# Performance work log

Measured on AMD Instinct MI355X. Metric: run time of the kernel, lower is better.

## Reference

```python
import jax, jax.numpy as jnp
import numpy as np

SOFTMAX_EPS = 1e-16  # PyG softmax denominator eps
LN_EPS = 1e-5
NEG_SLOPE = 0.2      # RGATConv default negative_slope
NUM_LAYERS = 4


def segment_softmax(alpha, seg, n):
    # softmax over edges sharing the same destination node ('across-relation')
    amax = jax.ops.segment_max(alpha, seg, num_segments=n)
    amax = jnp.where(jnp.isfinite(amax), amax, 0.0)
    e = jnp.exp(alpha - amax[seg])
    den = jax.ops.segment_sum(e, seg, num_segments=n)
    return e / (den[seg] + SOFTMAX_EPS)


def graph_layer_norm(x, w, b):
    # torch_geometric.nn.LayerNorm, mode='graph', batch=None:
    # normalize over ALL nodes and channels jointly
    mu = x.mean()
    xc = x - mu
    std = jnp.sqrt((xc * xc).mean())
    return xc / (std + LN_EPS) * w + b


def normalize_pos(pos):
    # NormalizeScale: center then scale so max |coord| ~ 1
    pos = pos - pos.mean(axis=0, keepdims=True)
    pos = pos * ((1.0 / jnp.abs(pos).max()) * 0.999999)
    # NormalizeRotation: rotate onto principal axes of pos^T pos
    c = pos.T @ pos  # (3,3)
    _, v = jnp.linalg.eigh(c)
    return pos @ v


def rgat_layer(x, src, dst, etype, W, q, k, bias, n):
    # RGATConv, heads=1, dim=1, concat=False, additive self-attention,
    # across-relation softmax, sum aggregation, eval mode (no dropout).
    # Transform per relation once: (R, N, O), then gather per edge.
    xr = jnp.einsum('nf,rfo->rno', x, W)
    out_j = xr[etype, src]            # (E, O) source messages
    out_i = xr[etype, dst]            # (E, O) target side
    qi = out_i @ q                    # (E, 1)
    kj = out_j @ k                    # (E, 1)
    alpha = jax.nn.leaky_relu(qi + kj, NEG_SLOPE)
    alpha = segment_softmax(alpha, dst, n)
    msg = alpha * out_j               # (E, O), heads=1 so mean over heads is identity
    agg = jax.ops.segment_sum(msg, dst, num_segments=n)
    return agg + bias


def setup_inputs() -> dict:
    key = jax.random.key(0)
    kk = jax.random.split(key, 16)
    N, E, R, IN, O, H2 = 100000, 3200000, 15, 35, 32, 256
    return {
        'data_batch_1': jax.random.normal(kk[0], (N, IN), jnp.float32),
        'data_batch_2': jax.random.normal(kk[1], (16, IN), jnp.float32),
        'edge_index_1': jax.random.randint(kk[2], (2, E), 0, N, jnp.int32),
        'edge_type_1': jax.random.randint(kk[3], (E,), 0, R, jnp.int32),
        'edge_index_2': jax.random.randint(kk[4], (2, 16), 0, 16, jnp.int32),
        'edge_type_2': jax.random.randint(kk[5], (16,), 0, R, jnp.int32),
        'W0': jax.random.normal(kk[6], (R, IN, O), jnp.float32) * 0.1,
        'q0': jax.random.normal(kk[7], (O, 1), jnp.float32) * 0.1,
        'k0': jax.random.normal(kk[8], (O, 1), jnp.float32) * 0.1,
        'b0': jnp.zeros((O,), jnp.float32),
        'Ws': jax.random.normal(kk[9], (NUM_LAYERS - 1, R, O, O), jnp.float32) * 0.1,
        'qs': jax.random.normal(kk[10], (NUM_LAYERS - 1, O, 1), jnp.float32) * 0.1,
        'ks': jax.random.normal(kk[11], (NUM_LAYERS - 1, O, 1), jnp.float32) * 0.1,
        'bs': jnp.zeros((NUM_LAYERS - 1, O), jnp.float32),
        'ln_w': jnp.ones((NUM_LAYERS, O), jnp.float32),
        'ln_b': jnp.zeros((NUM_LAYERS, O), jnp.float32),
        'ln1_w': jnp.ones((IN - 3,), jnp.float32),
        'ln1_b': jnp.zeros((IN - 3,), jnp.float32),
        'lin1_W': jax.random.normal(kk[12], (H2, O), jnp.float32) * 0.1,
        'lin1_b': jnp.zeros((H2,), jnp.float32),
    }


def reference(data_batch_1, data_batch_2, edge_index_1, edge_type_1,
              edge_index_2, edge_type_2,
              W0, q0, k0, b0, Ws, qs, ks, bs,
              ln_w, ln_b, ln1_w, ln1_b, lin1_W, lin1_b):
    n = data_batch_1.shape[0]
    xyz = normalize_pos(data_batch_1[:, :3])
    feats = graph_layer_norm(data_batch_1[:, 3:], ln1_w, ln1_b)
    x = jnp.concatenate([xyz, feats], axis=1)
    src, dst = edge_index_1[0], edge_index_1[1]
    prev = None
    for i in range(NUM_LAYERS):
        if i == 0:
            h = rgat_layer(x, src, dst, edge_type_1, W0, q0, k0, b0, n)
        else:
            h = rgat_layer(x, src, dst, edge_type_1,
                           Ws[i - 1], qs[i - 1], ks[i - 1], bs[i - 1], n)
        if prev is not None:  # residual from 2nd layer on
            h = h + prev
        h = graph_layer_norm(h, ln_w[i], ln_b[i])
        h = jax.nn.silu(h)
        prev = h
        x = h
    x3 = x.mean(axis=0)                                  # mean pool over nodes
    out = jax.nn.silu(x3 @ lin1_W.T + lin1_b)[None, :]   # (1, 256)
    # original returns (x, lins[-1]) which are the identical tensor
    return out
```

## Files before the change

kernel.cpp:

```cpp
#include <hip/hip_runtime.h>
#include <math.h>
#include <stdint.h>

#define NBLK 256

__device__ inline float bf2f(unsigned short u){
  union { unsigned int i; float f; } x; x.i = ((unsigned int)u) << 16; return x.f;
}
__device__ inline unsigned short f2bf(float f){
  union { float f; unsigned int i; } x; x.f = f;
  unsigned int u = x.i;
  return (unsigned short)((u + 0x7FFFu + ((u >> 16) & 1u)) >> 16);
}
__device__ inline float ldin(const void* p, size_t i, int f32){
  return f32 ? ((const float*)p)[i] : bf2f(((const unsigned short*)p)[i]);
}

__device__ inline int badf(float v){ return !(fabsf(v) <= 3.0e38f); }
__device__ inline int badd(double v){ return !(fabs(v) <= 1.0e300); }

__device__ inline double wsum_d(double v){
  #pragma unroll
  for (int o = 32; o > 0; o >>= 1) v += __shfl_down(v, o);
  return v;
}
__device__ inline double wmax_d(double v){
  #pragma unroll
  for (int o = 32; o > 0; o >>= 1) v = fmax(v, __shfl_down(v, o));
  return v;
}
__device__ inline void atomicMaxD(double* addr, double v){
  atomicMax((unsigned long long*)addr, (unsigned long long)__double_as_longlong(v));
}

typedef __attribute__((ext_vector_type(8))) short short8;
typedef __attribute__((ext_vector_type(4))) float f32x4;
__device__ inline f32x4 mfma16(short8 a, short8 b, f32x4 c){
  return __builtin_amdgcn_mfma_f32_16x16x32_bf16(a, b, c, 0, 0, 0);
}

__device__ inline double d_sign(double a, double b){ return (b >= 0.0) ? fabs(a) : -fabs(a); }
__device__ inline double dlapy2_(double x, double y){ return sqrt(x*x + y*y); }

__device__ void dlartg_(double f, double g, double* cs, double* sn, double* r){
  if (g == 0.0){ *cs = 1.0; *sn = 0.0; *r = f; }
  else if (f == 0.0){ *cs = 0.0; *sn = (g >= 0.0) ? 1.0 : -1.0; *r = fabs(g); }
  else {
    double d = sqrt(f*f + g*g);
    *cs = fabs(f)/d;
    *r  = d_sign(d, f);
    *sn = g / (*r);
  }
}

__device__ void dlaev2_(double a, double b, double c, double* rt1, double* rt2,
                        double* cs1, double* sn1){
  double sm = a + c, df = a - c, adf = fabs(df), tb = b + b, ab = fabs(tb);
  double acmx, acmn;
  if (fabs(a) > fabs(c)){ acmx = a; acmn = c; } else { acmx = c; acmn = a; }
  double rt;
  if (adf > ab) rt = adf*sqrt(1.0 + (ab/adf)*(ab/adf));
  else if (adf < ab) rt = ab*sqrt(1.0 + (adf/ab)*(adf/ab));
  else rt = ab*sqrt(2.0);
  int sgn1;
  if (sm < 0.0){ *rt1 = 0.5*(sm - rt); sgn1 = -1; *rt2 = (acmx/(*rt1))*acmn - (b/(*rt1))*b; }
  else if (sm > 0.0){ *rt1 = 0.5*(sm + rt); sgn1 = 1; *rt2 = (acmx/(*rt1))*acmn - (b/(*rt1))*b; }
  else { *rt1 = 0.5*rt; *rt2 = -0.5*rt; sgn1 = 1; }
  int sgn2; double cs;
  if (df >= 0.0){ cs = df + rt; sgn2 = 1; } else { cs = df - rt; sgn2 = -1; }
  double acs = fabs(cs);
  if (acs > ab){ double ct = -tb/cs; *sn1 = 1.0/sqrt(1.0+ct*ct); *cs1 = ct*(*sn1); }
  else {
    if (ab == 0.0){ *cs1 = 1.0; *sn1 = 0.0; }
    else { double tn = -cs/tb; *cs1 = 1.0/sqrt(1.0+tn*tn); *sn1 = tn*(*cs1); }
  }
  if (sgn1 == sgn2){ double tn = *cs1; *cs1 = -(*sn1); *sn1 = tn; }
}

__device__ void dsteqr3_(double* dd, double* ee, double z[3][3]){
  #define D_(i) dd[(i)-1]
  #define E_(i) ee[(i)-1]
  #define Z_(i,j) z[(i)-1][(j)-1]
  #define CW_(i) cw[(i)-1]
  #define SW_(i) sw[(i)-1]
  const int n = 3;
  const double eps = 1.1102230246251565e-16;
  const double eps2 = eps*eps;
  const double safmin = 2.2250738585072014e-308;
  const int nmaxit = n*30;
  double cw[3], sw[3];
  int jtot = 0;
  int l1 = 1, l, m, lsv, lend, lendsv;
  double p, g, r, c, s, f, b, rt1, rt2, anorm, tst;

L10:
  if (l1 > n) goto L160;
  if (l1 > 1) E_(l1-1) = 0.0;
  if (l1 <= n-1){
    for (m = l1; m <= n-1; ++m){
      tst = fabs(E_(m));
      if (tst == 0.0) goto L30;
      if (tst <= (sqrt(fabs(D_(m)))*sqrt(fabs(D_(m+1))))*eps){ E_(m) = 0.0; goto L30; }
    }
  }
  m = n;
L30:
  l = l1; lsv = l; lend = m; lendsv = lend; l1 = m+1;
  if (lend == l) goto L10;
  anorm = 0.0;
  for (int i = l; i <= lend; ++i) anorm = fmax(anorm, fabs(D_(i)));
  for (int i = l; i <= lend-1; ++i) anorm = fmax(anorm, fabs(E_(i)));
  if (anorm == 0.0) goto L10;
  if (fabs(D_(lend)) < fabs(D_(l))){ lend = lsv; l = lendsv; }
  if (lend > l) goto L40; else goto L90;

L40:
  if (l != lend){
    for (m = l; m <= lend-1; ++m){
      tst = fabs(E_(m)); tst = tst*tst;
      if (tst <= (eps2*fabs(D_(m)))*fabs(D_(m+1)) + safmin) goto L60;
    }
  }
  m = lend;
L60:
  if (m < lend) E_(m) = 0.0;
  p = D_(l);
  if (m == l) goto L80;
  if (m == l+1){
    dlaev2_(D_(l), E_(l), D_(l+1), &rt1, &rt2, &c, &s);
    CW_(l) = c; SW_(l) = s;
    { double ct = CW_(l), st = SW_(l);
      if (ct != 1.0 || st != 0.0)
        for (int i = 1; i <= n; ++i){
          double t = Z_(i, l+1);
          Z_(i, l+1) = ct*t - st*Z_(i, l);
          Z_(i, l)   = st*t + ct*Z_(i, l);
        }
    }
    D_(l) = rt1; D_(l+1) = rt2; E_(l) = 0.0;
    l += 2;
    if (l <= lend) goto L40;
    goto L140;
  }
  if (jtot == nmaxit) goto L140;
  jtot++;
  g = (D_(l+1) - p)/(2.0*E_(l));
  r = dlapy2_(g, 1.0);
  g = D_(m) - p + E_(l)/(g + d_sign(r, g));
  s = 1.0; c = 1.0; p = 0.0;
  for (int i = m-1; i >= l; --i){
    f = s*E_(i); b = c*E_(i);
    dlartg_(g, f, &c, &s, &r);
    if (i != m-1) E_(i+1) = r;
    g = D_(i+1) - p;
    r = (D_(i) - g)*s + 2.0*c*b;
    p = s*r;
    D_(i+1) = g + p;
    g = c*r - b;
    CW_(i) = c; SW_(i) = -s;
  }
  { int mm = m - l + 1;
    for (int j = mm-1; j >= 1; --j){
      double ct = CW_(l+j-1), st = SW_(l+j-1);
      if (ct != 1.0 || st != 0.0)
        for (int i = 1; i <= n; ++i){
          double t = Z_(i, l+j);
          Z_(i, l+j)   = ct*t - st*Z_(i, l+j-1);
          Z_(i, l+j-1) = st*t + ct*Z_(i, l+j-1);
        }
    }
  }
  D_(l) = D_(l) - p;
  E_(l) = g;
  goto L40;
L80:
  D_(l) = p;
  l++;
  if (l <= lend) goto L40;
  goto L140;

L90:
  if (l != lend){
    for (m = l; m >= lend+1; --m){
      tst = fabs(E_(m-1)); tst = tst*tst;
      if (tst <= (eps2*fabs(D_(m)))*fabs(D_(m-1)) + safmin) goto L110;
    }
  }
  m = lend;
L110:
  if (m > lend) E_(m-1) = 0.0;
  p = D_(l);
  if (m == l) goto L130;
  if (m == l-1){
    dlaev2_(D_(l-1), E_(l-1), D_(l), &rt1, &rt2, &c, &s);
    CW_(m) = c; SW_(m) = s;
    { double ct = CW_(m), st = SW_(m);
      if (ct != 1.0 || st != 0.0)
        for (int i = 1; i <= n; ++i){
          double t = Z_(i, l);
          Z_(i, l)   = ct*t - st*Z_(i, l-1);
          Z_(i, l-1) = st*t + ct*Z_(i, l-1);
        }
    }
    D_(l-1) = rt1; D_(l) = rt2; E_(l-1) = 0.0;
    l -= 2;
    if (l >= lend) goto L90;
    goto L140;
  }
  if (jtot == nmaxit) goto L140;
  jtot++;
  g = (D_(l-1) - p)/(2.0*E_(l-1));
  r = dlapy2_(g, 1.0);
  g = D_(m) - p + E_(l-1)/(g + d_sign(r, g));
  s = 1.0; c = 1.0; p = 0.0;
  for (int i = m; i <= l-1; ++i){
    f = s*E_(i); b = c*E_(i);
    dlartg_(g, f, &c, &s, &r);
    if (i != m) E_(i-1) = r;
    g = D_(i) - p;
    r = (D_(i+1) - g)*s + 2.0*c*b;
    p = s*r;
    D_(i) = g + p;
    g = c*r - b;
    CW_(i) = c; SW_(i) = s;
  }
  { int mm = l - m + 1;
    for (int j = 1; j <= mm-1; ++j){
      double ct = CW_(m+j-1), st = SW_(m+j-1);
      if (ct != 1.0 || st != 0.0)
        for (int i = 1; i <= n; ++i){
          double t = Z_(i, m+j);
          Z_(i, m+j)   = ct*t - st*Z_(i, m+j-1);
          Z_(i, m+j-1) = st*t + ct*Z_(i, m+j-1);
        }
    }
  }
  D_(l) = D_(l) - p;
  E_(l-1) = g;
  goto L90;
L130:
  D_(l) = p;
  l--;
  if (l >= lend) goto L90;
  goto L140;

L140:
  if (jtot < nmaxit) goto L10;
  goto L190;

L160:
  for (int ii = 2; ii <= n; ++ii){
    int i = ii-1, k = i;
    p = D_(i);
    for (int j = ii; j <= n; ++j) if (D_(j) < p){ k = j; p = D_(j); }
    if (k != i){
      D_(k) = D_(i); D_(i) = p;
      for (int rr = 1; rr <= n; ++rr){ double t = Z_(rr,i); Z_(rr,i) = Z_(rr,k); Z_(rr,k) = t; }
    }
  }
L190:
  ;
  #undef D_
  #undef E_
  #undef Z_
  #undef CW_
  #undef SW_
}

__device__ void eigh3_(const double C[3][3], double w[3], double v[3][3]){
  double a00=C[0][0], a10=C[1][0], a20=C[2][0], a11=C[1][1], a21=C[2][1], a22=C[2][2];
  double dd[3], ee[2], tau, v2;
  double alpha = a10, x = a20;
  double xnorm = fabs(x);
  if (xnorm == 0.0){ tau = 0.0; v2 = 0.0; ee[0] = alpha; }
  else {
    double beta = -d_sign(dlapy2_(alpha, xnorm), alpha);
    tau = (beta - alpha)/beta;
    v2 = x/(alpha - beta);
    ee[0] = beta;
  }
  if (tau != 0.0){
    double w0 = tau*(a11 + a21*v2);
    double w1 = tau*(a21 + a22*v2);
    double wv = w0 + w1*v2;
    double ac = -0.5*tau*wv;
    w0 += ac; w1 += ac*v2;
    a11 = a11 - 2.0*w0;
    a21 = a21 - (v2*w0 + w1);
    a22 = a22 - 2.0*v2*w1;
  }
  dd[0]=a00; dd[1]=a11; dd[2]=a22; ee[1]=a21;
  double z[3][3] = {{1,0,0},{0,1,0},{0,0,1}};
  dsteqr3_(dd, ee, z);
  for (int j = 0; j < 3; ++j){
    double t = z[1][j] + v2*z[2][j];
    z[1][j] -= tau*t;
    z[2][j] -= tau*t*v2;
  }
  for (int i=0;i<3;++i){ w[i]=dd[i]; for(int j=0;j<3;++j) v[i][j]=z[i][j]; }
}


__global__ void k_dtype(const unsigned short* __restrict__ data, int nus, double* PD){
  int* DF = (int*)(PD + 28);
  int t = threadIdx.x;
  int bad = 0;
  for (int i = t; i < nus; i += 256){
    int e = (data[i] >> 7) & 0xFF;
    if (e > 0x90 || (e && e < 0x60)) bad++;
  }
  #pragma unroll
  for (int o = 32; o > 0; o >>= 1) bad += __shfl_down(bad, o);
  __shared__ int sb[4];
  if ((t & 63) == 0) sb[t >> 6] = bad;
  __syncthreads();
  if (t == 0) DF[1] = ((sb[0]+sb[1]+sb[2]+sb[3]) > nus/16) ? 1 : 0;
}

__global__ void k_red1(const void* __restrict__ data, int N, double* PD){
  int n = blockIdx.x*blockDim.x + threadIdx.x;
  const int* DF = (const int*)(PD + 28);
  int f32 = DF[1];
  double v11[11] = {0,0,0,0,0,0,0,0,0,0,0};
  double m6[6] = {0,0,0,0,0,0};
  if (n < N){
    size_t rb = (size_t)n*35;
    double p0 = ldin(data, rb+0, f32);
    double p1 = ldin(data, rb+1, f32);
    double p2 = ldin(data, rb+2, f32);
    v11[0]=p0; v11[1]=p1; v11[2]=p2;
    double fs=0, fss=0;
    for (int k=3;k<35;++k){ double v = ldin(data, rb+k, f32); fs += v; fss += v*v; }
    v11[3]=fs; v11[4]=fss;
    v11[5]=p0*p0; v11[6]=p1*p0; v11[7]=p2*p0; v11[8]=p1*p1; v11[9]=p2*p1; v11[10]=p2*p2;
    m6[0]=64.0+p0; m6[1]=64.0+p1; m6[2]=64.0+p2;
    m6[3]=64.0-p0; m6[4]=64.0-p1; m6[5]=64.0-p2;
  }
  __shared__ double sred[17][4];
  int wid = threadIdx.x >> 6;
  int lane0 = ((threadIdx.x & 63) == 0);
  #pragma unroll
  for (int q=0;q<11;++q){
    double t = wsum_d(v11[q]);
    if (lane0) sred[q][wid] = t;
  }
  #pragma unroll
  for (int j=0;j<6;++j){
    double t = wmax_d(m6[j]);
    if (lane0) sred[11+j][wid] = t;
  }
  __syncthreads();
  int t = threadIdx.x;
  if (t < 11) atomicAdd(&PD[t], sred[t][0]+sred[t][1]+sred[t][2]+sred[t][3]);
  else if (t < 17)
    atomicMaxD(&PD[72+(t-11)],
      fmax(fmax(sred[t][0],sred[t][1]), fmax(sred[t][2],sred[t][3])));
}

__global__ void k_eig(double* PD, int N){
  if (threadIdx.x != 0 || blockIdx.x != 0) return;
  int* DF = (int*)(PD + 28);
  int bad0 = 0;
  for (int i=0;i<11;++i) if (badd(PD[i])) bad0 = 1;
  if (bad0) DF[0] |= 1;
  double dN = (double)N;
  double mu[3] = {PD[0]/dN, PD[1]/dN, PD[2]/dN};
  double amax = 0.0;
  for (int j=0;j<3;++j){
    double mx = (PD[72+j] - 64.0) - mu[j];
    double mnv = mu[j] - (64.0 - PD[75+j]);
    amax = fmax(amax, fmax(mx, mnv));
  }
  double s = 0.999999/amax;
  double s2 = s*s;
  double C[3][3];
  C[0][0]=(PD[5]-dN*mu[0]*mu[0])*s2; C[1][0]=(PD[6]-dN*mu[1]*mu[0])*s2;
  C[2][0]=(PD[7]-dN*mu[2]*mu[0])*s2; C[1][1]=(PD[8]-dN*mu[1]*mu[1])*s2;
  C[2][1]=(PD[9]-dN*mu[2]*mu[1])*s2; C[2][2]=(PD[10]-dN*mu[2]*mu[2])*s2;
  C[0][1]=C[1][0]; C[0][2]=C[2][0]; C[1][2]=C[2][1];
  double w[3], V[3][3];
  eigh3_(C, w, V);
  int bad1 = 0;
  for (int i=0;i<3;++i){ if (badd(w[i])) bad1=1; for (int j=0;j<3;++j) if (badd(V[i][j])) bad1=1; }
  if (bad1){
    DF[0] |= 2;
    for (int i=0;i<3;++i) for (int j=0;j<3;++j) V[i][j] = (i==j) ? 1.0 : 0.0;
  }
  PD[12]=mu[0]; PD[13]=mu[1]; PD[14]=mu[2];
  PD[15]=s;
  for (int i=0;i<3;++i) for (int j=0;j<3;++j) PD[16+i*3+j]=V[i][j];
  double cntf = dN*32.0;
  double mu1 = PD[3]/cntf;
  double var = PD[4]/cntf - mu1*mu1;
  PD[25]=mu1;
  PD[26]=1.0/(sqrt(var>0.0?var:0.0)+1e-5);
}

__global__ void k_buildx(const void* __restrict__ data,
                         const void* __restrict__ ln1w,
                         const void* __restrict__ ln1b,
                         double* __restrict__ PD, float* __restrict__ x, int N){
  int n = blockIdx.x*blockDim.x + threadIdx.x;
  if (n >= N) return;
  int* DF = (int*)(PD + 28);
  int f32 = DF[1];
  size_t rb = (size_t)n*35;
  double s = PD[15];
  double p0 = ((double)ldin(data, rb+0, f32) - PD[12])*s;
  double p1 = ((double)ldin(data, rb+1, f32) - PD[13])*s;
  double p2 = ((double)ldin(data, rb+2, f32) - PD[14])*s;
  float* xr = x + (size_t)n*36;
  int bb = 0;
  for (int j=0;j<3;++j){
    float v = (float)(p0*PD[16+j] + p1*PD[19+j] + p2*PD[22+j]);
    bb |= badf(v);
    xr[j] = v;
  }
  float mu1 = (float)PD[25], rs = (float)PD[26];
  for (int k=0;k<32;++k){
    float v = (ldin(data, rb+3+k, f32) - mu1)*rs*ldin(ln1w, k, f32) + ldin(ln1b, k, f32);
    bb |= badf(v);
    xr[3+k] = v;
  }
  xr[35] = 0.f;
  if (bb) atomicOr(DF, 4);
}

__global__ void k_count(const int* __restrict__ dst, int* __restrict__ cnt, int E){
  int i = blockIdx.x*blockDim.x + threadIdx.x;
  if (i < E) atomicAdd(&cnt[dst[i]], 1);
}

__global__ void k_scan1(const int* __restrict__ cnt, int* __restrict__ bsum, int N){
  int i = blockIdx.x*256 + threadIdx.x;
  int v = (i < N) ? cnt[i] : 0;
  #pragma unroll
  for (int o=32;o>0;o>>=1) v += __shfl_down(v, o);
  __shared__ int s4[4];
  if ((threadIdx.x&63)==0) s4[threadIdx.x>>6]=v;
  __syncthreads();
  if (threadIdx.x==0) bsum[blockIdx.x]=s4[0]+s4[1]+s4[2]+s4[3];
}

__global__ void k_scan2(const int* __restrict__ bsum, int* __restrict__ bpre,
                        int* __restrict__ iptr, int nb, int N){
  if (threadIdx.x != 0 || blockIdx.x != 0) return;
  int run = 0;
  for (int b=0;b<nb;++b){ bpre[b]=run; run += bsum[b]; }
  iptr[N] = run;
}

__global__ void k_scan3(const int* __restrict__ cnt, const int* __restrict__ bpre,
                        int* __restrict__ iptr, int* __restrict__ cur, int N){
  __shared__ int sc[256];
  int i = blockIdx.x*256 + threadIdx.x;
  int t = threadIdx.x;
  int v = (i < N) ? cnt[i] : 0;
  sc[t] = v;
  __syncthreads();
  for (int o=1;o<256;o<<=1){
    int add = (t >= o) ? sc[t-o] : 0;
    __syncthreads();
    sc[t] += add;
    __syncthreads();
  }
  if (i < N){
    int val = bpre[blockIdx.x] + sc[t] - v;
    iptr[i] = val;
    cur[i] = val;
  }
}

__global__ void k_hist(const int* __restrict__ dst, int* __restrict__ H,
                       int E, int per, int nb){
  __shared__ int lc[256];
  int blk = blockIdx.x, t = threadIdx.x;
  lc[t] = 0;
  __syncthreads();
  int s = blk*per, e = min(E, s+per);
  for (int i = s+t; i < e; i += 256) atomicAdd(&lc[dst[i] >> 9], 1);
  __syncthreads();
  if (t < nb) H[t*NBLK + blk] = lc[t];
}

__global__ void k_xscan(const int* __restrict__ H, const int* __restrict__ iptr,
                        int* __restrict__ offs){
  __shared__ int sc[256];
  int b = blockIdx.x, t = threadIdx.x;
  int v = H[b*NBLK + t];
  sc[t] = v;
  __syncthreads();
  for (int o=1;o<256;o<<=1){
    int add = (t >= o) ? sc[t-o] : 0;
    __syncthreads();
    sc[t] += add;
    __syncthreads();
  }
  offs[b*NBLK + t] = iptr[b << 9] + sc[t] - v;
}

__global__ void k_binA2(const int* __restrict__ src, const int* __restrict__ dst,
                        const int* __restrict__ et, const int* __restrict__ offs,
                        int* __restrict__ stag, int E, int per){
  __shared__ int lc[256];
  int blk = blockIdx.x, t = threadIdx.x;
  lc[t] = 0;
  __syncthreads();
  int s = blk*per, e = min(E, s+per);
  for (int i = s+t; i < e; i += 256){
    int d = dst[i];
    int b = d >> 9;
    int r = atomicAdd(&lc[b], 1);
    stag[offs[b*NBLK + blk] + r] = src[i] | (et[i] << 17) | ((d & 511) << 21);
  }
}

__global__ void k_binB2(const int* __restrict__ iptr, const int* __restrict__ stag,
                        int* __restrict__ pack, int N){
  __shared__ int lcnt[512];
  int b = blockIdx.x;
  int n0 = b << 9;
  int t = threadIdx.x;
  for (int j = t; j < 512; j += 256){
    int n = n0 + j;
    lcnt[j] = (n < N) ? iptr[n] : 0;
  }
  __syncthreads();
  int segs = iptr[n0];
  int nend = (n0 + 512 < N) ? (n0 + 512) : N;
  int sege = iptr[nend];
  for (int k = segs + t; k < sege; k += 256){
    int e2 = stag[k];
    int pos = atomicAdd(&lcnt[(e2 >> 21) & 511], 1);
    pack[pos] = (e2 & 0x1FFFF) | (((e2 >> 17) & 15) << 20);
  }
}

__global__ void k_scatter(const int* __restrict__ src, const int* __restrict__ dst,
                          const int* __restrict__ et, int* __restrict__ cur,
                          int* __restrict__ pack, int E){
  int i = blockIdx.x*blockDim.x + threadIdx.x;
  if (i < E){
    int d = dst[i];
    int p = atomicAdd(&cur[d], 1);
    pack[p] = src[i] | (et[i] << 20);
  }
}

__global__ void k_fragpack(const void* __restrict__ W, size_t wofs, int F, int KC,
                           const void* __restrict__ qp, const void* __restrict__ kp,
                           size_t qofs,
                           unsigned short* __restrict__ bfr,
                           unsigned short* __restrict__ qkfr,
                           const int* __restrict__ DF){
  int t = blockIdx.x*blockDim.x + threadIdx.x;
  int nB = 15*KC*2*64*8;
  int nQ = 2*2*KC*64*8;
  int f32 = DF[1];
  if (t < nB){
    int j = t & 7; int lane = (t >> 3) & 63; int tile = (t >> 9) & 1; int idx = t >> 10;
    int kc = idx % KC; int r = idx / KC;
    int f = kc*32 + (lane >> 4)*8 + j;
    int o = tile*16 + (lane & 15);
    bfr[t] = (f < F) ? f2bf(ldin(W, wofs + ((size_t)(r*F+f))*32 + o, f32)) : 0;
  } else if (t < nB + nQ){
    int u = t - nB;
    int j = u & 7; int lane = (u >> 3) & 63; int wpk = u >> 9;
    int kc = wpk % KC; int wp = wpk / KC;
    int part = wp & 1; int which = wp >> 1;
    int f = kc*32 + (lane >> 4)*8 + j;
    int rr = lane & 15;
    unsigned short val = 0;
    if (f < F && rr < 15){
      const void* v = which ? kp : qp;
      float acc = 0.f;
      for (int o = 0; o < 32; ++o)
        acc = fmaf(ldin(W, wofs + ((size_t)(rr*F+f))*32 + o, f32), ldin(v, qofs + o, f32), acc);
      unsigned short hi = f2bf(acc);
      val = (part == 0) ? hi : f2bf(acc - bf2f(hi));
    }
    qkfr[u] = val;
  }
}

__global__ void __launch_bounds__(256)
k_mf(const float* __restrict__ x, int str, int KC, int N,
     const unsigned short* __restrict__ bfr,
     const unsigned short* __restrict__ qkfr,
     unsigned short* __restrict__ y, float* __restrict__ yq, float* __restrict__ yk){
  int wave = blockIdx.x*(blockDim.x >> 6) + (threadIdx.x >> 6);
  int node0 = wave*16;
  if (node0 >= N) return;
  int lane = threadIdx.x & 63;
  int col = lane & 15, quad = lane >> 4;
  int r0 = blockIdx.y*3;

  short8 ah[2], al[2];
  #pragma unroll
  for (int kc = 0; kc < 2; ++kc){
    if (kc >= KC) break;
    float xv[8];
    int node = node0 + col;
    int kbase = kc*32 + quad*8;
    if (node < N && kbase < str){
      const float* xr = x + (size_t)node*str + kbase;
      if (kbase + 8 <= str){
        float4 a = *(const float4*)xr; float4 b = *(const float4*)(xr + 4);
        xv[0]=a.x; xv[1]=a.y; xv[2]=a.z; xv[3]=a.w; xv[4]=b.x; xv[5]=b.y; xv[6]=b.z; xv[7]=b.w;
      } else if (kbase + 4 <= str){
        float4 a = *(const float4*)xr;
        xv[0]=a.x; xv[1]=a.y; xv[2]=a.z; xv[3]=a.w; xv[4]=0.f; xv[5]=0.f; xv[6]=0.f; xv[7]=0.f;
      } else {
        #pragma unroll
        for (int j=0;j<8;++j) xv[j]=0.f;
      }
    } else {
      #pragma unroll
      for (int j=0;j<8;++j) xv[j]=0.f;
    }
    #pragma unroll
    for (int j=0;j<8;++j){
      unsigned short hi = f2bf(xv[j]);
      ah[kc][j] = (short)hi;
      al[kc][j] = (short)f2bf(xv[j] - bf2f(hi));
    }
  }

  const short8* B  = (const short8*)bfr;
  const short8* QK = (const short8*)qkfr;

  if (blockIdx.y == 0){
    f32x4 aq = {0.f,0.f,0.f,0.f}, ak2 = {0.f,0.f,0.f,0.f};
    for (int kc = 0; kc < KC; ++kc){
      short8 qh = QK[((0*KC) + kc)*64 + lane];
      short8 ql = QK[((1*KC) + kc)*64 + lane];
      short8 kh = QK[((2*KC) + kc)*64 + lane];
      short8 kl = QK[((3*KC) + kc)*64 + lane];
      aq = mfma16(ah[kc], qh, aq);
      aq = mfma16(al[kc], qh, aq);
      aq = mfma16(ah[kc], ql, aq);
      ak2 = mfma16(ah[kc], kh, ak2);
      ak2 = mfma16(al[kc], kh, ak2);
      ak2 = mfma16(ah[kc], kl, ak2);
    }
    #pragma unroll
    for (int j = 0; j < 4; ++j){
      int node = node0 + quad*4 + j;
      if (node < N){
        yq[(size_t)node*16 + col] = aq[j];
        yk[(size_t)node*16 + col] = ak2[j];
      }
    }
  }

  for (int r = r0; r < r0+3; ++r){
    f32x4 a0 = {0.f,0.f,0.f,0.f}, a1 = {0.f,0.f,0.f,0.f};
    for (int kc = 0; kc < KC; ++kc){
      short8 b0 = B[(((size_t)(r*KC + kc))*2 + 0)*64 + lane];
      short8 b1 = B[(((size_t)(r*KC + kc))*2 + 1)*64 + lane];
      a0 = mfma16(ah[kc], b0, a0);
      a0 = mfma16(al[kc], b0, a0);
      a1 = mfma16(ah[kc], b1, a1);
      a1 = mfma16(al[kc], b1, a1);
    }
    #pragma unroll
    for (int j = 0; j < 4; ++j){
      int node = node0 + quad*4 + j;
      if (node < N){
        unsigned int pk = (unsigned int)f2bf(a0[j]) | ((unsigned int)f2bf(a1[j]) << 16);
        *(unsigned int*)&y[(((size_t)r*N + node))*32 + col*2] = pk;
      }
    }
  }
}

__global__ void k_main(const int* __restrict__ iptr, const int* __restrict__ pack,
                       const float* __restrict__ yq, const float* __restrict__ yk,
                       const unsigned short* __restrict__ y,
                       const void* __restrict__ biasp, size_t bofs,
                       const float* __restrict__ xres, float* __restrict__ hpre,
                       double* __restrict__ partials, int* __restrict__ DF, int N){
  __shared__ double sdb[4][2];
  int gt = blockIdx.x*blockDim.x + threadIdx.x;
  int node = gt >> 6, lane = gt & 63;
  int wid = threadIdx.x >> 6;
  int f32 = DF[1];
  int o = lane & 31;
  int os = ((o & 15) << 1) | (o >> 4);
  bool active = (node < N);
  float hp = 0.f;

  if (active){
    int start = iptr[node];
    int deg = iptr[node+1] - start;
    const float* yqn = yq + (size_t)node*16;
    float acc = 0.f;
    float ssum = 0.f;

    if (deg <= 64){
      int pe = 0; float a = -INFINITY;
      if (lane < deg){
        pe = pack[start+lane];
        int sr = pe & 0xFFFFF, et = pe >> 20;
        a = yqn[et] + yk[(size_t)sr*16+et];
        a = (a >= 0.f) ? a : 0.2f*a;
      }
      float amax = a;
      #pragma unroll
      for (int o2=32;o2>0;o2>>=1) amax = fmaxf(amax, __shfl_xor(amax, o2));
      float ev = (lane < deg) ? expf(a - amax) : 0.f;
      ssum = ev;
      int sub = lane >> 5;
      for (; sub + 14 < deg; sub += 16){
        float w0 = __shfl(ev, sub),    w1 = __shfl(ev, sub+2);
        float w2 = __shfl(ev, sub+4),  w3 = __shfl(ev, sub+6);
        float w4 = __shfl(ev, sub+8),  w5 = __shfl(ev, sub+10);
        float w6 = __shfl(ev, sub+12), w7 = __shfl(ev, sub+14);
        int   p0 = __shfl(pe, sub),    p1 = __shfl(pe, sub+2);
        int   p2 = __shfl(pe, sub+4),  p3 = __shfl(pe, sub+6);
        int   p4 = __shfl(pe, sub+8),  p5 = __shfl(pe, sub+10);
        int   p6 = __shfl(pe, sub+12), p7 = __shfl(pe, sub+14);
        float v0 = bf2f(y[((size_t)(p0 >> 20)*N + (p0 & 0xFFFFF))*32 + os]);
        float v1 = bf2f(y[((size_t)(p1 >> 20)*N + (p1 & 0xFFFFF))*32 + os]);
        float v2 = bf2f(y[((size_t)(p2 >> 20)*N + (p2 & 0xFFFFF))*32 + os]);
        float v3 = bf2f(y[((size_t)(p3 >> 20)*N + (p3 & 0xFFFFF))*32 + os]);
        float v4 = bf2f(y[((size_t)(p4 >> 20)*N + (p4 & 0xFFFFF))*32 + os]);
        float v5 = bf2f(y[((size_t)(p5 >> 20)*N + (p5 & 0xFFFFF))*32 + os]);
        float v6 = bf2f(y[((size_t)(p6 >> 20)*N + (p6 & 0xFFFFF))*32 + os]);
        float v7 = bf2f(y[((size_t)(p7 >> 20)*N + (p7 & 0xFFFFF))*32 + os]);
        acc = fmaf(w0, v0, acc); acc = fmaf(w1, v1, acc);
        acc = fmaf(w2, v2, acc); acc = fmaf(w3, v3, acc);
        acc = fmaf(w4, v4, acc); acc = fmaf(w5, v5, acc);
        acc = fmaf(w6, v6, acc); acc = fmaf(w7, v7, acc);
      }
      for (; sub + 6 < deg; sub += 8){
        float w0 = __shfl(ev, sub),   w1 = __shfl(ev, sub+2);
        float w2 = __shfl(ev, sub+4), w3 = __shfl(ev, sub+6);
        int   p0 = __shfl(pe, sub),   p1 = __shfl(pe, sub+2);
        int   p2 = __shfl(pe, sub+4), p3 = __shfl(pe, sub+6);
        float v0 = bf2f(y[((size_t)(p0 >> 20)*N + (p0 & 0xFFFFF))*32 + os]);
        float v1 = bf2f(y[((size_t)(p1 >> 20)*N + (p1 & 0xFFFFF))*32 + os]);
        float v2 = bf2f(y[((size_t)(p2 >> 20)*N + (p2 & 0xFFFFF))*32 + os]);
        float v3 = bf2f(y[((size_t)(p3 >> 20)*N + (p3 & 0xFFFFF))*32 + os]);
        acc = fmaf(w0, v0, acc); acc = fmaf(w1, v1, acc);
        acc = fmaf(w2, v2, acc); acc = fmaf(w3, v3, acc);
      }
      for (; sub < deg; sub += 2){
        float wgt = __shfl(ev, sub);
        int pb = __shfl(pe, sub);
        acc = fmaf(wgt, bf2f(y[((size_t)(pb >> 20)*N + (pb & 0xFFFFF))*32 + os]), acc);
      }
    } else {
      float amax = -INFINITY;
      for (int k = lane; k < deg; k += 64){
        int pe = pack[start+k];
        int sr = pe & 0xFFFFF, et = pe >> 20;
        float a = yqn[et] + yk[(size_t)sr*16+et];
        a = (a >= 0.f) ? a : 0.2f*a;
        amax = fmaxf(amax, a);
      }
      #pragma unroll
      for (int o2=32;o2>0;o2>>=1) amax = fmaxf(amax, __shfl_xor(amax, o2));
      for (int c = 0; c < deg; c += 64){
        int k = c + lane;
        float ev = 0.f; int pe = 0;
        if (k < deg){
          pe = pack[start+k];
          int sr = pe & 0xFFFFF, et = pe >> 20;
          float a = yqn[et] + yk[(size_t)sr*16+et];
          a = (a >= 0.f) ? a : 0.2f*a;
          ev = expf(a - amax);
          ssum += ev;
        }
        int lim = min(64, deg - c);
        int sub = lane >> 5;
        for (; sub + 6 < lim; sub += 8){
          float w0 = __shfl(ev, sub),   w1 = __shfl(ev, sub+2);
          float w2 = __shfl(ev, sub+4), w3 = __shfl(ev, sub+6);
          int   p0 = __shfl(pe, sub),   p1 = __shfl(pe, sub+2);
          int   p2 = __shfl(pe, sub+4), p3 = __shfl(pe, sub+6);
          float v0 = bf2f(y[((size_t)(p0 >> 20)*N + (p0 & 0xFFFFF))*32 + os]);
          float v1 = bf2f(y[((size_t)(p1 >> 20)*N + (p1 & 0xFFFFF))*32 + os]);
          float v2 = bf2f(y[((size_t)(p2 >> 20)*N + (p2 & 0xFFFFF))*32 + os]);
          float v3 = bf2f(y[((size_t)(p3 >> 20)*N + (p3 & 0xFFFFF))*32 + os]);
          acc = fmaf(w0, v0, acc);
          acc = fmaf(w1, v1, acc);
          acc = fmaf(w2, v2, acc);
          acc = fmaf(w3, v3, acc);
        }
        for (; sub < lim; sub += 2){
          float wgt = __shfl(ev, sub);
          int pb = __shfl(pe, sub);
          acc = fmaf(wgt, bf2f(y[((size_t)(pb >> 20)*N + (pb & 0xFFFFF))*32 + os]), acc);
        }
      }
    }
    #pragma unroll
    for (int o2=32;o2>0;o2>>=1) ssum += __shfl_xor(ssum, o2);
    float inv = 1.f/(ssum + 1e-16f);
    acc *= inv;
    acc += __shfl_xor(acc, 32);

    if (lane < 32){
      hp = acc + ldin(biasp, bofs + o, f32);
      if (xres) hp += xres[(size_t)node*32 + o];
      if (badf(hp)) atomicOr(DF, 32);
      hpre[(size_t)node*32 + o] = hp;
    }
  }

  float s1 = (active && lane < 32) ? hp : 0.f;
  float s2 = s1*s1;
  #pragma unroll
  for (int o2=32;o2>0;o2>>=1){ s1 += __shfl_xor(s1,o2); s2 += __shfl_xor(s2,o2); }
  if (lane == 0){ sdb[wid][0] = (double)s1; sdb[wid][1] = (double)s2; }
  __syncthreads();
  if (threadIdx.x == 0){
    partials[(size_t)blockIdx.x*2]   = sdb[0][0]+sdb[1][0]+sdb[2][0]+sdb[3][0];
    partials[(size_t)blockIdx.x*2+1] = sdb[0][1]+sdb[1][1]+sdb[2][1]+sdb[3][1];
  }
}

__global__ void k_stat(const double* __restrict__ partials, int nb,
                       double* __restrict__ PD, int l){
  double t1 = 0.0, t2 = 0.0;
  for (int i = threadIdx.x; i < nb; i += 256){
    t1 += partials[(size_t)i*2];
    t2 += partials[(size_t)i*2+1];
  }
  t1 = wsum_d(t1); t2 = wsum_d(t2);
  __shared__ double sd[8];
  int w = threadIdx.x >> 6;
  if ((threadIdx.x & 63) == 0){ sd[w*2] = t1; sd[w*2+1] = t2; }
  __syncthreads();
  if (threadIdx.x == 0){
    PD[32+2*l]   = sd[0]+sd[2]+sd[4]+sd[6];
    PD[32+2*l+1] = sd[1]+sd[3]+sd[5]+sd[7];
  }
}

__global__ void k_ln(float* __restrict__ h, const void* __restrict__ lnw,
                     const void* __restrict__ lnb, size_t lofs,
                     double* __restrict__ PD, int l, int N){
  int idx = blockIdx.x*blockDim.x + threadIdx.x;
  if (idx >= N*32) return;
  int* DF = (int*)(PD + 28);
  int f32 = DF[1];
  const double* stats = PD + 32 + 2*l;
  int o = idx & 31;
  double cntf = (double)N*32.0;
  double mu = stats[0]/cntf;
  double var = stats[1]/cntf - mu*mu;
  float rstd = (float)(1.0/(sqrt(var>0.0?var:0.0) + 1e-5));
  float v = (h[idx] - (float)mu)*rstd*ldin(lnw, lofs + o, f32) + ldin(lnb, lofs + o, f32);
  v = v / (1.f + expf(-v));
  if (badf(v)) atomicOr(DF, 64);
  h[idx] = v;
}

__global__ void k_pool(const float* __restrict__ h, double* __restrict__ PD, int N){
  __shared__ float sp[8][33];
  int t = threadIdx.x, o = t & 31, g = t >> 5;
  int r0 = blockIdx.x*256;
  float s = 0.f;
  for (int r = r0 + g; r < N && r < r0 + 256; r += 8) s += h[(size_t)r*32 + o];
  sp[g][o] = s;
  __syncthreads();
  if (t < 32){
    float tot = 0.f;
    #pragma unroll
    for (int g2=0; g2<8; ++g2) tot += sp[g2][t];
    atomicAdd(&PD[40 + t], (double)tot);
  }
}

__global__ void k_out(double* __restrict__ PD, const void* __restrict__ Wl,
                      const void* __restrict__ bl, void* __restrict__ out, int N, int H2){
  int j = blockIdx.x*blockDim.x + threadIdx.x;
  if (j >= H2) return;
  int* DF = (int*)(PD + 28);
  int f32 = DF[1];
  int flag = DF[0];
  const double* pool = PD + 40;
  float acc = ldin(bl, j, f32);
  for (int o=0;o<32;++o)
    acc = fmaf((float)(pool[o]/(double)N), ldin(Wl, (size_t)j*32+o, f32), acc);
  if (badf(acc)) flag |= 128;
  float v = acc / (1.f + expf(-acc));
  if (flag) v = (float)flag;
  if (f32) ((float*)out)[j] = v;
  else     ((unsigned short*)out)[j] = f2bf(v);
}

__global__ void k_diag(unsigned short* out, float val, int H2){
  int j = blockIdx.x*blockDim.x + threadIdx.x;
  if (j < H2) out[j] = f2bf(val);
}

extern "C" void kernel_launch(void* const* d_in, const int* in_sizes, int n_in,
                              void* d_out, int out_size, void* d_ws, size_t ws_size,
                              hipStream_t stream)
{
  const int N  = in_sizes[0] / 35;
  const int E  = in_sizes[3];
  const int R  = 15;
  const int H2 = in_sizes[19];

  const void* data = d_in[0];
  const int* ei  = (const int*)d_in[2];
  const int* etp = (const int*)d_in[3];
  const void* W0  = d_in[6];
  const void* q0  = d_in[7];
  const void* k0  = d_in[8];
  const void* b0  = d_in[9];
  const void* Wsp = d_in[10];
  const void* qsp = d_in[11];
  const void* ksp = d_in[12];
  const void* bsp = d_in[13];
  const void* lnw = d_in[14];
  const void* lnb = d_in[15];
  const void* ln1w= d_in[16];
  const void* ln1b= d_in[17];
  const void* l1W = d_in[18];
  const void* l1b = d_in[19];

  char* base = (char*)d_ws;
  size_t off = 0;
  auto A = [&](size_t nb)->size_t { size_t c = off; off += (nb + 255) & ~(size_t)255; return c; };
  size_t oPD  = A(1024);
  size_t oCnt = A((size_t)N*4);
  size_t oPtr = A(((size_t)N+1)*4);
  size_t oCur = A((size_t)N*4);
  size_t oBs  = A(4096);
  size_t oBp  = A(4096);
  size_t oPk  = A((size_t)E*4);
  size_t oSt  = A((size_t)E*4);
  size_t oHh  = A((size_t)256*NBLK*4);
  size_t oOf  = A((size_t)256*NBLK*4);
  size_t oX   = A((size_t)N*36*4);
  size_t oH0  = A((size_t)N*32*4);
  size_t oH1  = A((size_t)N*32*4);
  size_t oYq  = A((size_t)N*16*4);
  size_t oYk  = A((size_t)N*16*4);
  size_t oBf  = A((size_t)15*2*2*64*8*2);
  size_t oQk  = A((size_t)2*2*2*64*8*2);
  int nbMain  = (int)(((size_t)N*64 + 255)/256);
  size_t oPt  = A((size_t)nbMain*2*8);
  size_t oY   = off;
  size_t needB = oY + (size_t)R*N*32*2;

  double* PD  = (double*)(base + oPD);
  int* DF     = (int*)(PD + 28);
  int* cnt    = (int*)(base + oCnt);
  int* iptr   = (int*)(base + oPtr);
  int* cur    = (int*)(base + oCur);
  int* bsum   = (int*)(base + oBs);
  int* bpre   = (int*)(base + oBp);
  int* pack   = (int*)(base + oPk);
  int* stag   = (int*)(base + oSt);
  int* Hh     = (int*)(base + oHh);
  int* offs   = (int*)(base + oOf);
  float* xb   = (float*)(base + oX);
  float* h0   = (float*)(base + oH0);
  float* h1   = (float*)(base + oH1);
  float* yqb  = (float*)(base + oYq);
  float* ykb  = (float*)(base + oYk);
  unsigned short* bfr  = (unsigned short*)(base + oBf);
  unsigned short* qkfr = (unsigned short*)(base + oQk);
  double* partials = (double*)(base + oPt);
  unsigned short* y = (unsigned short*)(base + oY);

  if (ws_size < needB){
    k_diag<<<1, 256, 0, stream>>>((unsigned short*)d_out, (float)(ws_size >> 20), H2);
    return;
  }

  hipMemsetAsync(base, 0, oPtr, stream);

  int nbN = (N + 255)/256;
  int nbE = (E + 255)/256;
  int nus = (in_sizes[0] < 1024) ? in_sizes[0] : 1024;

  k_dtype<<<1, 256, 0, stream>>>((const unsigned short*)data, nus, PD);
  k_red1<<<nbN, 256, 0, stream>>>(data, N, PD);
  k_eig<<<1, 1, 0, stream>>>(PD, N);
  k_buildx<<<nbN, 256, 0, stream>>>(data, ln1w, ln1b, PD, xb, N);

  k_count<<<nbE, 256, 0, stream>>>(ei + E, cnt, E);
  k_scan1<<<nbN, 256, 0, stream>>>(cnt, bsum, N);
  k_scan2<<<1, 1, 0, stream>>>(bsum, bpre, iptr, nbN, N);
  k_scan3<<<nbN, 256, 0, stream>>>(cnt, bpre, iptr, cur, N);

  if (N <= (1 << 17)){
    int nbkt = (N + 511) >> 9;
    int per  = (E + NBLK - 1) / NBLK;
    k_hist<<<NBLK, 256, 0, stream>>>(ei + E, Hh, E, per, nbkt);
    k_xscan<<<nbkt, 256, 0, stream>>>(Hh, iptr, offs);
    k_binA2<<<NBLK, 256, 0, stream>>>(ei, ei + E, etp, offs, stag, E, per);
    k_binB2<<<nbkt, 256, 0, stream>>>(iptr, stag, pack, N);
  } else {
    k_scatter<<<nbE, 256, 0, stream>>>(ei, ei + E, etp, cur, pack, E);
  }

  int nbMf = (int)(((N + 15)/16 + 3)/4);
  for (int l=0; l<4; ++l){
    const void* W  = (l==0)? W0 : Wsp;  size_t wofs = (l==0)? 0 : (size_t)(l-1)*R*32*32;
    const void* qp = (l==0)? q0 : qsp;  size_t qofs = (l==0)? 0 : (size_t)(l-1)*32;
    const void* kp = (l==0)? k0 : ksp;
    const void* bp = (l==0)? b0 : bsp;  size_t bofs = qofs;
    int str = (l==0)? 36 : 32;
    int KC = (l==0)? 2 : 1;
    int F = (l==0)? 35 : 32;
    const float* xin = (l==0)? xb : ((l%2==0)? h1 : h0);
    float* hout = (l%2==0)? h0 : h1;
    int nFrag = 15*KC*2*64*8 + 2*2*KC*64*8;
    k_fragpack<<<(nFrag+255)/256, 256, 0, stream>>>(W, wofs, F, KC, qp, kp, qofs, bfr, qkfr, DF);
    dim3 gmf((unsigned)nbMf, 5);
    k_mf<<<gmf, 256, 0, stream>>>(xin, str, KC, N, bfr, qkfr, y, yqb, ykb);
    k_main<<<nbMain, 256, 0, stream>>>(iptr, pack, yqb, ykb, y, bp, bofs,
                 (l==0)? (const float*)nullptr : xin, hout, partials, DF, N);
    k_stat<<<1, 256, 0, stream>>>(partials, nbMain, PD, l);
    k_ln<<<(N*32+255)/256, 256, 0, stream>>>(hout, lnw, lnb, (size_t)l*32, PD, l, N);
  }

  k_pool<<<nbN, 256, 0, stream>>>(h1, PD, N);
  k_out<<<(H2+255)/256, 256, 0, stream>>>(PD, l1W, l1b, d_out, N, H2);
}
```

Measured before the change: 1.345 ms.

## Derive CSR row pointers from bucket histogram, dropping global per-node count pass

The separate per-node degree count (a global atomic pass over all edges) and the three-kernel scan are removed from the small-N path. Bucket totals now come from the existing block histogram and are scanned into bucket bases. The second binning kernel counts each node's edges in shared memory, scans them locally, and writes the CSR row pointers itself. This removes an E-sized pass with global atomics, at the cost of reading the staging buffer twice in the final binning kernel.

New measurement: 1.217 ms. -9.5%, faster.

```diff
diff --git a/kernel.cpp b/kernel.cpp
--- a/kernel.cpp
+++ b/kernel.cpp
@@ -471,71 +471,6 @@
   }
 }
 
-__global__ void k_hist(const int* __restrict__ dst, int* __restrict__ H,
-                       int E, int per, int nb){
-  __shared__ int lc[256];
-  int blk = blockIdx.x, t = threadIdx.x;
-  lc[t] = 0;
-  __syncthreads();
-  int s = blk*per, e = min(E, s+per);
-  for (int i = s+t; i < e; i += 256) atomicAdd(&lc[dst[i] >> 9], 1);
-  __syncthreads();
-  if (t < nb) H[t*NBLK + blk] = lc[t];
-}
-
-__global__ void k_xscan(const int* __restrict__ H, const int* __restrict__ iptr,
-                        int* __restrict__ offs){
-  __shared__ int sc[256];
-  int b = blockIdx.x, t = threadIdx.x;
-  int v = H[b*NBLK + t];
-  sc[t] = v;
-  __syncthreads();
-  for (int o=1;o<256;o<<=1){
-    int add = (t >= o) ? sc[t-o] : 0;
-    __syncthreads();
-    sc[t] += add;
-    __syncthreads();
-  }
-  offs[b*NBLK + t] = iptr[b << 9] + sc[t] - v;
-}
-
-__global__ void k_binA2(const int* __restrict__ src, const int* __restrict__ dst,
-                        const int* __restrict__ et, const int* __restrict__ offs,
-                        int* __restrict__ stag, int E, int per){
-  __shared__ int lc[256];
-  int blk = blockIdx.x, t = threadIdx.x;
-  lc[t] = 0;
-  __syncthreads();
-  int s = blk*per, e = min(E, s+per);
-  for (int i = s+t; i < e; i += 256){
-    int d = dst[i];
-    int b = d >> 9;
-    int r = atomicAdd(&lc[b], 1);
-    stag[offs[b*NBLK + blk] + r] = src[i] | (et[i] << 17) | ((d & 511) << 21);
-  }
-}
-
-__global__ void k_binB2(const int* __restrict__ iptr, const int* __restrict__ stag,
-                        int* __restrict__ pack, int N){
-  __shared__ int lcnt[512];
-  int b = blockIdx.x;
-  int n0 = b << 9;
-  int t = threadIdx.x;
-  for (int j = t; j < 512; j += 256){
-    int n = n0 + j;
-    lcnt[j] = (n < N) ? iptr[n] : 0;
-  }
-  __syncthreads();
-  int segs = iptr[n0];
-  int nend = (n0 + 512 < N) ? (n0 + 512) : N;
-  int sege = iptr[nend];
-  for (int k = segs + t; k < sege; k += 256){
-    int e2 = stag[k];
-    int pos = atomicAdd(&lcnt[(e2 >> 21) & 511], 1);
-    pack[pos] = (e2 & 0x1FFFF) | (((e2 >> 17) & 15) << 20);
-  }
-}
-
 __global__ void k_scatter(const int* __restrict__ src, const int* __restrict__ dst,
                           const int* __restrict__ et, int* __restrict__ cur,
                           int* __restrict__ pack, int E){
@@ -544,6 +479,115 @@
     int d = dst[i];
     int p = atomicAdd(&cur[d], 1);
     pack[p] = src[i] | (et[i] << 20);
+  }
+}
+
+__global__ void k_hist(const int* __restrict__ dst, int* __restrict__ H,
+                       int E, int per, int nb){
+  __shared__ int lc[256];
+  int blk = blockIdx.x, t = threadIdx.x;
+  lc[t] = 0;
+  __syncthreads();
+  int s = blk*per, e = min(E, s+per);
+  for (int i = s+t; i < e; i += 256) atomicAdd(&lc[dst[i] >> 9], 1);
+  __syncthreads();
+  if (t < nb) H[t*NBLK + blk] = lc[t];
+}
+
+__global__ void k_bsum1(const int* __restrict__ H, int* __restrict__ btot){
+  int b = blockIdx.x;
+  int v = H[b*NBLK + threadIdx.x];
+  #pragma unroll
+  for (int o=32;o>0;o>>=1) v += __shfl_down(v, o);
+  __shared__ int s4[4];
+  if ((threadIdx.x&63)==0) s4[threadIdx.x>>6]=v;
+  __syncthreads();
+  if (threadIdx.x==0) btot[b]=s4[0]+s4[1]+s4[2]+s4[3];
+}
+
+__global__ void k_bpre(const int* __restrict__ btot, int* __restrict__ bbase, int nbkt){
+  __shared__ int sc[256];
+  int t = threadIdx.x;
+  int v = (t < nbkt) ? btot[t] : 0;
+  sc[t] = v;
+  __syncthreads();
+  for (int o=1;o<256;o<<=1){
+    int add = (t >= o) ? sc[t-o] : 0;
+    __syncthreads();
+    sc[t] += add;
+    __syncthreads();
+  }
+  if (t <= nbkt && t < 256) bbase[t] = (t == 0) ? 0 : sc[t-1];
+  if (t == 0 && nbkt == 256) bbase[256] = sc[255];
+}
+
+__global__ void k_xscan(const int* __restrict__ H, const int* __restrict__ bbase,
+                        int* __restrict__ offs){
+  __shared__ int sc[256];
+  int b = blockIdx.x, t = threadIdx.x;
+  int v = H[b*NBLK + t];
+  sc[t] = v;
+  __syncthreads();
+  for (int o=1;o<256;o<<=1){
+    int add = (t >= o) ? sc[t-o] : 0;
+    __syncthreads();
+    sc[t] += add;
+    __syncthreads();
+  }
+  offs[b*NBLK + t] = bbase[b] + sc[t] - v;
+}
+
+__global__ void k_binA2(const int* __restrict__ src, const int* __restrict__ dst,
+                        const int* __restrict__ et, const int* __restrict__ offs,
+                        int* __restrict__ stag, int E, int per){
+  __shared__ int lc[256];
+  int blk = blockIdx.x, t = threadIdx.x;
+  lc[t] = 0;
+  __syncthreads();
+  int s = blk*per, e = min(E, s+per);
+  for (int i = s+t; i < e; i += 256){
+    int d = dst[i];
+    int b = d >> 9;
+    int r = atomicAdd(&lc[b], 1);
+    stag[offs[b*NBLK + blk] + r] = src[i] | (et[i] << 17) | ((d & 511) << 21);
+  }
+}
+
+__global__ void k_binB3(const int* __restrict__ bbase, const int* __restrict__ stag,
+                        int* __restrict__ pack, int* __restrict__ iptr,
+                        int N, int E, int nbkt){
+  __shared__ int lcnt[512];
+  __shared__ int ssum[256];
+  int b = blockIdx.x;
+  int n0 = b << 9;
+  int t = threadIdx.x;
+  lcnt[t] = 0; lcnt[t+256] = 0;
+  __syncthreads();
+  int segs = bbase[b], sege = bbase[b+1];
+  for (int k = segs + t; k < sege; k += 256)
+    atomicAdd(&lcnt[(stag[k] >> 21) & 511], 1);
+  __syncthreads();
+  int c0 = lcnt[2*t], c1 = lcnt[2*t+1];
+  int s = c0 + c1;
+  ssum[t] = s;
+  __syncthreads();
+  for (int o=1;o<256;o<<=1){
+    int add = (t >= o) ? ssum[t-o] : 0;
+    __syncthreads();
+    ssum[t] += add;
+    __syncthreads();
+  }
+  int p0 = segs + ssum[t] - s;
+  int p1 = p0 + c0;
+  lcnt[2*t] = p0; lcnt[2*t+1] = p1;
+  if (n0 + 2*t < N)     iptr[n0 + 2*t]     = p0;
+  if (n0 + 2*t+1 < N)   iptr[n0 + 2*t+1]   = p1;
+  if (b == nbkt-1 && t == 0) iptr[N] = E;
+  __syncthreads();
+  for (int k = segs + t; k < sege; k += 256){
+    int e2 = stag[k];
+    int pos = atomicAdd(&lcnt[(e2 >> 21) & 511], 1);
+    pack[pos] = (e2 & 0x1FFFF) | (((e2 >> 17) & 15) << 20);
   }
 }
 
@@ -933,6 +977,8 @@
   size_t oCur = A((size_t)N*4);
   size_t oBs  = A(4096);
   size_t oBp  = A(4096);
+  size_t oBb  = A(2048);
+  size_t oBt  = A(2048);
   size_t oPk  = A((size_t)E*4);
   size_t oSt  = A((size_t)E*4);
   size_t oHh  = A((size_t)256*NBLK*4);
@@ -956,6 +1002,8 @@
   int* cur    = (int*)(base + oCur);
   int* bsum   = (int*)(base + oBs);
   int* bpre   = (int*)(base + oBp);
+  int* bbase  = (int*)(base + oBb);
+  int* btot   = (int*)(base + oBt);
   int* pack   = (int*)(base + oPk);
   int* stag   = (int*)(base + oSt);
   int* Hh     = (int*)(base + oHh);
@@ -986,19 +1034,20 @@
   k_eig<<<1, 1, 0, stream>>>(PD, N);
   k_buildx<<<nbN, 256, 0, stream>>>(data, ln1w, ln1b, PD, xb, N);
 
-  k_count<<<nbE, 256, 0, stream>>>(ei + E, cnt, E);
-  k_scan1<<<nbN, 256, 0, stream>>>(cnt, bsum, N);
-  k_scan2<<<1, 1, 0, stream>>>(bsum, bpre, iptr, nbN, N);
-  k_scan3<<<nbN, 256, 0, stream>>>(cnt, bpre, iptr, cur, N);
-
   if (N <= (1 << 17)){
     int nbkt = (N + 511) >> 9;
     int per  = (E + NBLK - 1) / NBLK;
     k_hist<<<NBLK, 256, 0, stream>>>(ei + E, Hh, E, per, nbkt);
-    k_xscan<<<nbkt, 256, 0, stream>>>(Hh, iptr, offs);
+    k_bsum1<<<nbkt, 256, 0, stream>>>(Hh, btot);
+    k_bpre<<<1, 256, 0, stream>>>(btot, bbase, nbkt);
+    k_xscan<<<nbkt, 256, 0, stream>>>(Hh, bbase, offs);
     k_binA2<<<NBLK, 256, 0, stream>>>(ei, ei + E, etp, offs, stag, E, per);
-    k_binB2<<<nbkt, 256, 0, stream>>>(iptr, stag, pack, N);
+    k_binB3<<<nbkt, 256, 0, stream>>>(bbase, stag, pack, iptr, N, E, nbkt);
   } else {
+    k_count<<<nbE, 256, 0, stream>>>(ei + E, cnt, E);
+    k_scan1<<<nbN, 256, 0, stream>>>(cnt, bsum, N);
+    k_scan2<<<1, 1, 0, stream>>>(bsum, bpre, iptr, nbN, N);
+    k_scan3<<<nbN, 256, 0, stream>>>(cnt, bpre, iptr, cur, N);
     k_scatter<<<nbE, 256, 0, stream>>>(ei, ei + E, etp, cur, pack, E);
   }
 
```
